# Kernel tuning notes

Measured on AMD Instinct MI355X. Metric: run time of the kernel, lower is better.

Reference implementation:

```python
import jax, jax.numpy as jnp
import numpy as np

T, B = 128, 512
OBS_DIM = 512
HIDDEN = 512
ACTION_DIM = 18
LN_EPS = 1e-6  # flax LayerNorm default


def _layer_norm(x, scale, bias):
    m = jnp.mean(x, axis=-1, keepdims=True)
    v = jnp.var(x, axis=-1, keepdims=True)
    return (x - m) * jax.lax.rsqrt(v + LN_EPS) * scale + bias


def setup_inputs() -> dict:
    key = jax.random.key(0)
    ks = jax.random.split(key, 16)
    sc = lambda k, sh: jax.random.normal(k, sh, jnp.float32) * (1.0 / np.sqrt(sh[0]))
    d = {}
    d['hidden'] = jax.random.normal(ks[0], (B, HIDDEN), jnp.float32)
    d['obs'] = jax.random.normal(ks[1], (T, B, OBS_DIM), jnp.float32)
    d['dones'] = jax.random.randint(ks[2], (T, B), 0, 2).astype(bool)
    d['last_acts'] = jax.random.randint(ks[3], (T, B), 0, ACTION_DIM, dtype=jnp.int32)
    in0 = OBS_DIM + ACTION_DIM
    d['w0'] = sc(ks[4], (in0, HIDDEN)); d['b0'] = jnp.zeros((HIDDEN,), jnp.float32)
    d['ln0_s'] = jnp.ones((HIDDEN,), jnp.float32); d['ln0_b'] = jnp.zeros((HIDDEN,), jnp.float32)
    d['w1'] = sc(ks[5], (HIDDEN, HIDDEN)); d['b1'] = jnp.zeros((HIDDEN,), jnp.float32)
    d['ln1_s'] = jnp.ones((HIDDEN,), jnp.float32); d['ln1_b'] = jnp.zeros((HIDDEN,), jnp.float32)
    d['w_ir'] = sc(ks[6], (HIDDEN, HIDDEN)); d['b_ir'] = jnp.zeros((HIDDEN,), jnp.float32)
    d['w_iz'] = sc(ks[7], (HIDDEN, HIDDEN)); d['b_iz'] = jnp.zeros((HIDDEN,), jnp.float32)
    d['w_in'] = sc(ks[8], (HIDDEN, HIDDEN)); d['b_in'] = jnp.zeros((HIDDEN,), jnp.float32)
    d['w_hr'] = sc(ks[9], (HIDDEN, HIDDEN))
    d['w_hz'] = sc(ks[10], (HIDDEN, HIDDEN))
    d['w_hn'] = sc(ks[11], (HIDDEN, HIDDEN)); d['b_hn'] = jnp.zeros((HIDDEN,), jnp.float32)
    d['w_out'] = sc(ks[12], (HIDDEN, ACTION_DIM)); d['b_out'] = jnp.zeros((ACTION_DIM,), jnp.float32)
    return d


def reference(hidden, obs, dones, last_acts,
              w0, b0, ln0_s, ln0_b, w1, b1, ln1_s, ln1_b,
              w_ir, b_ir, w_iz, b_iz, w_in, b_in,
              w_hr, w_hz, w_hn, b_hn, w_out, b_out):
    # embed last actions and concat with obs: [T, B, obs_dim + action_dim]
    one_hot = jax.nn.one_hot(last_acts, ACTION_DIM, dtype=obs.dtype)
    x = jnp.concatenate([obs, one_hot], axis=-1)
    # MLP encoder: Dense -> LayerNorm -> relu, applied over all (T, B) at once
    x = jax.nn.relu(_layer_norm(x @ w0 + b0, ln0_s, ln0_b))
    x = jax.nn.relu(_layer_norm(x @ w1 + b1, ln1_s, ln1_b))

    # ScannedRNN: GRUCell with reset-to-zero carry on done, scanned over time
    def step(h, xs):
        xt, dt = xs  # xt: [B, H], dt: [B] bool
        h = jnp.where(dt[:, None], jnp.zeros_like(h), h)
        r = jax.nn.sigmoid(xt @ w_ir + b_ir + h @ w_hr)
        z = jax.nn.sigmoid(xt @ w_iz + b_iz + h @ w_hz)
        n = jnp.tanh(xt @ w_in + b_in + r * (h @ w_hn + b_hn))
        h_new = (1.0 - z) * n + z * h
        return h_new, h_new

    new_hidden, y = jax.lax.scan(step, hidden, (x, dones))
    q_vals = y @ w_out + b_out  # [T, B, action_dim]
    return new_hidden, q_vals
```

## Files before the change

### kernel.cpp

```cpp
#include <hip/hip_runtime.h>
#include <cstdint>
#include <cstddef>


#define TT 128
#define BBATCH 512
#define HH 512
#define MM 65536
#define AD 18
#define GSTEPS 8
#define FSTRIDE 32
#define READY_U32 1064960

typedef __attribute__((ext_vector_type(8))) short short8;
typedef __attribute__((ext_vector_type(4))) float float4v;
typedef __attribute__((ext_vector_type(4))) unsigned int uint4v;

__device__ __forceinline__ unsigned short f2bf(float f) {
  union { float f; unsigned int u; } v; v.f = f;
  unsigned int r = v.u + 0x7fffu + ((v.u >> 16) & 1u);
  return (unsigned short)(r >> 16);
}
__device__ __forceinline__ float bf2f(unsigned short h) {
  union { unsigned int u; float f; } v; v.u = ((unsigned int)h) << 16;
  return v.f;
}

__device__ __forceinline__ unsigned int load_u32_coh(const unsigned int* p) {
  unsigned int v;
  asm volatile("global_load_dword %0, %1, off sc0 sc1\n\ts_waitcnt vmcnt(0)"
               : "=v"(v) : "v"(p) : "memory");
  return v;
}
__device__ __forceinline__ void store_u32_coh(unsigned int* p, unsigned int v) {
  asm volatile("global_store_dword %0, %1, off sc0 sc1"
               :: "v"(p), "v"(v) : "memory");
}
__device__ __forceinline__ void store_u64_coh(void* p, unsigned long long v) {
  asm volatile("global_store_dwordx2 %0, %1, off sc0 sc1"
               :: "v"(p), "v"(v) : "memory");
}

typedef __attribute__((address_space(3))) unsigned int* lds_u32p;
typedef const __attribute__((address_space(1))) unsigned int* glb_u32p;
__device__ __forceinline__ void async16(void* lds, const void* g) {
  __builtin_amdgcn_global_load_lds(
      (glb_u32p)(unsigned long long)g,
      (lds_u32p)(unsigned int)(unsigned long long)lds, 16, 0, 0);
}


__global__ __launch_bounds__(256) void k_prep(
    const float* __restrict__ w0, const float* __restrict__ w1,
    const float* __restrict__ wir, const float* __restrict__ wiz,
    const float* __restrict__ win,
    const float* __restrict__ whr, const float* __restrict__ whz,
    const float* __restrict__ whn,
    const float* __restrict__ bir, const float* __restrict__ biz,
    const float* __restrict__ bin, const float* __restrict__ wout,
    const float* __restrict__ hidden, const int* __restrict__ dI,
    unsigned short* __restrict__ W0at, unsigned short* __restrict__ W1t,
    unsigned short* __restrict__ Wit, unsigned short* __restrict__ Whf,
    unsigned short* __restrict__ w0act, float* __restrict__ gib,
    unsigned short* __restrict__ WoutT, unsigned short* __restrict__ hbuf,
    unsigned int* __restrict__ flag) {
  int i = blockIdx.x * 256 + threadIdx.x;
  if (i < 1310720) {
    int o = i & 262143, z = i >> 18;
    int n = o >> 9, k = o & 511;
    const float* s = (z == 0) ? w0 : (z == 1) ? w1 : (z == 2) ? wir
                   : (z == 3) ? wiz : win;
    unsigned short b = f2bf(s[k * 512 + n]);
    if (z == 0) W0at[o] = b;
    else if (z == 1) W1t[o] = b;
    else Wit[(size_t)(z - 2) * 262144 + o] = b;
  } else if (i < 2097152) {
    int j = i - 1310720;
    int k = j / 1536, n = j - k * 1536;
    const float* s = (n < 512) ? whr : (n < 1024) ? whz : whn;
    Whf[((size_t)(k >> 3) * 1536 + n) * 8 + (k & 7)] = f2bf(s[k * 512 + (n & 511)]);
  } else {
    int j = i - 2097152;
    if (j < 9216) {
      int a = j >> 9, n = j & 511;
      w0act[j] = f2bf(w0[(512 + a) * 512 + n]);
    }
    if (j < 1536)
      gib[j] = (j < 512) ? bir[j] : (j < 1024) ? biz[j - 512] : bin[j - 1024];
    if (j < 32768) {
      int n = j >> 9, k = j & 511;
      WoutT[j] = f2bf(n < AD ? wout[k * AD + n] : 0.f);
    }
    hbuf[j] = f2bf(hidden[j]);
  }
  if (blockIdx.x == 9215) {
    __shared__ int wany[4];
    int t = threadIdx.x;
    int any = 0;
#pragma unroll 8
    for (int v = 0; v < 64; ++v) any |= dI[t * 64 + v] & 0xFFFFFFFE;
    unsigned long long b = __ballot(any != 0);
    if ((t & 63) == 0) wany[t >> 6] = (b != 0ull) ? 1 : 0;
    __syncthreads();
    if (t == 0) *flag = (unsigned int)(wany[0] | wany[1] | wany[2] | wany[3]);
  }
}

__global__ __launch_bounds__(256) void k_zero(unsigned int* __restrict__ p) {
  int i = (blockIdx.x * 256 + threadIdx.x) * 4;
  if (i < READY_U32) *(uint4v*)(p + i) = (uint4v){0u, 0u, 0u, 0u};
}


template <int MODE>
__global__ __launch_bounds__(512, 1) void k_enc(
    const unsigned short* __restrict__ Ab,
    const unsigned short* __restrict__ Btb,
    unsigned short* __restrict__ Cb,
    const float* __restrict__ bias,
    const float* __restrict__ lnS, const float* __restrict__ lnB,
    const unsigned short* __restrict__ gW,
    const int* __restrict__ acts) {
  __shared__ __align__(16) unsigned char AsRaw[MODE == 0 ? 32768 : 16384];
  __shared__ unsigned short Bs[32768];
  __shared__ float part[128][4][2];
  __shared__ float stats[128][2];
  float* Asf = (float*)AsRaw;
  unsigned short* Ash = (unsigned short*)AsRaw;

  const int tid = threadIdx.x, wave = tid >> 6, lane = tid & 63;
  const int quad = lane >> 4, l15 = lane & 15;
  const int wm = wave >> 2, wn = wave & 3;
  const int m0 = blockIdx.x * 128;
  const int g = (MODE == 2) ? blockIdx.y : 0;
  const unsigned short* Bt = Btb + (size_t)g * 262144;
  const float* bi = bias + g * 512;

  float4v acc[4][8];
#pragma unroll
  for (int a = 0; a < 4; ++a)
#pragma unroll
    for (int b = 0; b < 8; ++b) acc[a][b] = (float4v){0.f, 0.f, 0.f, 0.f};

  for (int k0 = 0; k0 < 512; k0 += 64) {
    if constexpr (MODE == 0) {
      const float* Af = (const float*)Ab;
#pragma unroll
      for (int r = 0; r < 4; ++r) {
        int u = r * 512 + tid;
        int ch = u >> 8, rem = u & 255, mm = rem >> 1, half = rem & 1;
        async16(&Asf[(size_t)(r * 512 + wave * 64) * 4],
                Af + (size_t)(m0 + mm) * 512 + k0 + ch * 8 + half * 4);
      }
    } else {
#pragma unroll
      for (int r = 0; r < 2; ++r) {
        int u = r * 512 + tid;
        int ch = u >> 7, mm = u & 127;
        async16(&Ash[(size_t)(r * 512 + wave * 64) * 8],
                Ab + (size_t)(m0 + mm) * 512 + k0 + ch * 8);
      }
    }
#pragma unroll
    for (int r = 0; r < 8; ++r) {
      int u = r * 512 + tid;
      int ch = u >> 9, nn = u & 511;
      async16(&Bs[(size_t)(r * 512 + wave * 64) * 8],
              Bt + (size_t)nn * 512 + k0 + ch * 8);
    }
    __syncthreads();
#pragma unroll
    for (int kk = 0; kk < 2; ++kk) {
      short8 afr[4], bfr[8];
#pragma unroll
      for (int mi = 0; mi < 4; ++mi) {
        int mrow = wm * 64 + mi * 16 + l15;
        if constexpr (MODE == 0) {
          const float* ap = &Asf[(size_t)((kk * 4 + quad) * 128 + mrow) * 8];
          float4v lo = *(const float4v*)ap;
          float4v hi = *(const float4v*)(ap + 4);
          short8 f;
#pragma unroll
          for (int j = 0; j < 4; ++j) {
            f[j] = (short)f2bf(lo[j]);
            f[j + 4] = (short)f2bf(hi[j]);
          }
          afr[mi] = f;
        } else {
          afr[mi] = *(const short8*)
              &Ash[(size_t)((kk * 4 + quad) * 128 + mrow) * 8];
        }
      }
#pragma unroll
      for (int ni = 0; ni < 8; ++ni)
        bfr[ni] = *(const short8*)
            &Bs[((kk * 4 + quad) * 512 + wn * 128 + ni * 16 + l15) * 8];
#pragma unroll
      for (int mi = 0; mi < 4; ++mi)
#pragma unroll
        for (int ni = 0; ni < 8; ++ni)
          acc[mi][ni] = __builtin_amdgcn_mfma_f32_16x16x32_bf16(
              afr[mi], bfr[ni], acc[mi][ni], 0, 0, 0);
    }
    __syncthreads();
  }

  float bcol[8];
#pragma unroll
  for (int ni = 0; ni < 8; ++ni) bcol[ni] = bi[wn * 128 + ni * 16 + l15];
#pragma unroll
  for (int mi = 0; mi < 4; ++mi)
#pragma unroll
    for (int i = 0; i < 4; ++i) {
      int row = m0 + wm * 64 + mi * 16 + quad * 4 + i;
      int arow = (MODE == 0) ? acts[row] : 0;
#pragma unroll
      for (int ni = 0; ni < 8; ++ni) {
        float v = acc[mi][ni][i] + bcol[ni];
        if (MODE == 0) v += bf2f(gW[arow * 512 + wn * 128 + ni * 16 + l15]);
        acc[mi][ni][i] = v;
      }
    }

  if (MODE <= 1) {
#pragma unroll
    for (int mi = 0; mi < 4; ++mi)
#pragma unroll
      for (int i = 0; i < 4; ++i) {
        float s = 0.f, q = 0.f;
#pragma unroll
        for (int ni = 0; ni < 8; ++ni) {
          float v = acc[mi][ni][i];
          s += v; q += v * v;
        }
#pragma unroll
        for (int d = 1; d < 16; d <<= 1) {
          s += __shfl_xor(s, d, 64);
          q += __shfl_xor(q, d, 64);
        }
        if (l15 == 0) {
          int rowl = wm * 64 + mi * 16 + quad * 4 + i;
          part[rowl][wn][0] = s;
          part[rowl][wn][1] = q;
        }
      }
    __syncthreads();
    if (tid < 128) {
      float s = part[tid][0][0] + part[tid][1][0] + part[tid][2][0] + part[tid][3][0];
      float q = part[tid][0][1] + part[tid][1][1] + part[tid][2][1] + part[tid][3][1];
      float mean = s * (1.f / 512.f);
      float var = fmaxf(q * (1.f / 512.f) - mean * mean, 0.f);
      stats[tid][0] = mean;
      stats[tid][1] = rsqrtf(var + 1e-6f);
    }
    __syncthreads();
    float sc8[8], cb8[8];
#pragma unroll
    for (int ni = 0; ni < 8; ++ni) {
      int col = wn * 128 + ni * 16 + l15;
      sc8[ni] = lnS[col];
      cb8[ni] = lnB[col];
    }
#pragma unroll
    for (int mi = 0; mi < 4; ++mi)
#pragma unroll
      for (int i = 0; i < 4; ++i) {
        int rowl = wm * 64 + mi * 16 + quad * 4 + i;
        float mean = stats[rowl][0], rstd = stats[rowl][1];
        int row = m0 + rowl;
#pragma unroll
        for (int ni = 0; ni < 8; ++ni) {
          int col = wn * 128 + ni * 16 + l15;
          float v = fmaxf((acc[mi][ni][i] - mean) * rstd * sc8[ni] + cb8[ni], 0.f);
          Cb[(size_t)row * 512 + col] = f2bf(v);
        }
      }
  } else {
#pragma unroll
    for (int mi = 0; mi < 4; ++mi)
#pragma unroll
      for (int i = 0; i < 4; ++i) {
        int row = m0 + wm * 64 + mi * 16 + quad * 4 + i;
        int t = row >> 9, b = row & 511;
#pragma unroll
        for (int ni = 0; ni < 8; ++ni) {
          int c = wn * 128 + ni * 16 + l15;
          size_t dst = ((size_t)((b >> 5) * 16 + (c >> 5)) * 128 + t) * 3072
                     + (size_t)g * 1024 + (b & 31) * 32 + (c & 31);
          Cb[dst] = f2bf(acc[mi][ni][i]);
        }
      }
  }
}


__global__ __launch_bounds__(256, 1) void k_gru(
    const unsigned short* __restrict__ Whf, const unsigned short* __restrict__ gin,
    const float* __restrict__ bhn, const int* __restrict__ dI,
    const unsigned char* __restrict__ dB, const unsigned int* __restrict__ flag,
    const unsigned short* __restrict__ hbuf, unsigned short* __restrict__ ybuf,
    float* __restrict__ outh, unsigned int* __restrict__ ready) {
  __shared__ __align__(16) unsigned short gin_lds[2][GSTEPS * 3 * 32 * 32];
  __shared__ unsigned char d_lds[TT * 32];

  const int tid = threadIdx.x, wave = tid >> 6, lane = tid & 63;
  const int quad = lane >> 4, l15 = lane & 15;
  const int rt = blockIdx.x & 15;
  const int cc = blockIdx.x >> 4;
  const int r0b = rt * 32;
  const int rowb = (wave & 1) * 16 + l15;
  const int row = r0b + rowb;
  const int c0 = cc * 32 + (wave >> 1) * 16 + quad * 4;
  const int bytemode = (int)(*flag);
  const float4v bhn4 = *(const float4v*)(bhn + c0);

  const unsigned short* gsrc = gin + (size_t)(rt * 16 + cc) * 128 * 3072;

  auto stage_gin = [&](int buf, int t0) {
    const unsigned short* src = gsrc + (size_t)t0 * 3072;
#pragma unroll
    for (int r = 0; r < 12; ++r) {
      async16(&gin_lds[buf][(size_t)(r * 256 + wave * 64) * 8],
              src + (size_t)(r * 256 + tid) * 8);
    }
  };

  stage_gin(0, 0);
#pragma unroll
  for (int r = 0; r < 16; ++r) {
    int idx = r * 256 + tid;
    int t = idx >> 5, rr = idx & 31;
    int gidx = t * 512 + r0b + rr;
    d_lds[idx] = bytemode ? dB[gidx] : (unsigned char)(dI[gidx] != 0);
  }

  short8 bw[3][16];
#pragma unroll
  for (int kc = 0; kc < 16; ++kc)
#pragma unroll
    for (int g = 0; g < 3; ++g) {
      size_t u = (size_t)(kc * 4 + quad) * 1536
               + (g * 512 + cc * 32 + (wave >> 1) * 16 + l15);
      bw[g][kc] = *(const short8*)(Whf + u * 8);
    }

  float hprev[4];
  {
    unsigned long long w = *(const unsigned long long*)(hbuf + (size_t)row * 512 + c0);
#pragma unroll
    for (int i = 0; i < 4; ++i) hprev[i] = bf2f((unsigned short)(w >> (16 * i)));
  }

  __syncthreads();

  for (int t = 0; t < TT; ++t) {
    if (t > 0) {
      if (wave == 0) {
        const unsigned int* fp =
            ready + (((size_t)rt * 130 + t) * 16 + (lane & 15)) * FSTRIDE;
        unsigned int v;
        int guard = 0;
        do {
          v = load_u32_coh(fp);
        } while (__ballot(v == 0u) != 0ull && ++guard < (1 << 22));
      }
      __syncthreads();
      asm volatile("" ::: "memory");
    }

    const unsigned short* hsrc =
        (t == 0) ? hbuf : ybuf + (size_t)(t - 1) * 262144;
    const unsigned short* ap = hsrc + (size_t)row * 512 + quad * 8;
    short8 af[16];
#pragma unroll
    for (int kc = 0; kc < 16; ++kc) af[kc] = *(const short8*)(ap + kc * 32);

    const int dd = (int)d_lds[(t << 5) + rowb];
    if (dd) {
      const short8 z8 = {0, 0, 0, 0, 0, 0, 0, 0};
#pragma unroll
      for (int kc = 0; kc < 16; ++kc) af[kc] = z8;
    }

    if ((t & (GSTEPS - 1)) == 0 && t + GSTEPS < TT)
      stage_gin(((t >> 3) + 1) & 1, t + GSTEPS);

    const int sl = t & (GSTEPS - 1), bufc = (t >> 3) & 1;
    float gr[4], gz[4], gn[4];
    {
      const unsigned short* gl = &gin_lds[bufc][(size_t)sl * 3072
          + rowb * 32 + (wave >> 1) * 16 + quad * 4];
      unsigned long long w0 = *(const unsigned long long*)(gl);
      unsigned long long w1 = *(const unsigned long long*)(gl + 1024);
      unsigned long long w2 = *(const unsigned long long*)(gl + 2048);
#pragma unroll
      for (int i = 0; i < 4; ++i) {
        gr[i] = bf2f((unsigned short)(w0 >> (16 * i)));
        gz[i] = bf2f((unsigned short)(w1 >> (16 * i)));
        gn[i] = bf2f((unsigned short)(w2 >> (16 * i)));
      }
    }

    float4v a0 = {0.f, 0.f, 0.f, 0.f}, a1 = a0, a2 = a0;
#pragma unroll
    for (int kc = 0; kc < 16; ++kc) {
      a0 = __builtin_amdgcn_mfma_f32_16x16x32_bf16(bw[0][kc], af[kc], a0, 0, 0, 0);
      a1 = __builtin_amdgcn_mfma_f32_16x16x32_bf16(bw[1][kc], af[kc], a1, 0, 0, 0);
      a2 = __builtin_amdgcn_mfma_f32_16x16x32_bf16(bw[2][kc], af[kc], a2, 0, 0, 0);
    }

    unsigned short* ydst = ybuf + (size_t)t * 262144;
    float hv[4];
#pragma unroll
    for (int i = 0; i < 4; ++i) {
      float hold = dd ? 0.f : hprev[i];
      float r = 1.f / (1.f + __expf(-(a0[i] + gr[i])));
      float z = 1.f / (1.f + __expf(-(a1[i] + gz[i])));
      float npre = gn[i] + r * (a2[i] + bhn4[i]);
      float n = 1.f - 2.f / (1.f + __expf(2.f * npre));
      hv[i] = (1.f - z) * n + z * hold;
      hprev[i] = hv[i];
    }
    {
      unsigned long long pk = (unsigned long long)f2bf(hv[0])
          | ((unsigned long long)f2bf(hv[1]) << 16)
          | ((unsigned long long)f2bf(hv[2]) << 32)
          | ((unsigned long long)f2bf(hv[3]) << 48);
      store_u64_coh(ydst + (size_t)row * 512 + c0, pk);
    }
    if (t == TT - 1) {
      float4v o = {hv[0], hv[1], hv[2], hv[3]};
      *(float4v*)(outh + (size_t)row * 512 + c0) = o;
    }

    __syncthreads();
    if (tid == 0)
      store_u32_coh(&ready[(((size_t)rt * 130 + t + 1) * 16 + cc) * FSTRIDE], 1u);
  }
}


__global__ __launch_bounds__(256) void k_qout(
    const unsigned short* __restrict__ Yb, const unsigned short* __restrict__ Wt,
    const float* __restrict__ bout, float* __restrict__ Q) {
  __shared__ unsigned short As[8192];
  __shared__ unsigned short Bs[4096];
  const int tid = threadIdx.x, wave = tid >> 6, lane = tid & 63;
  const int quad = lane >> 4, l15 = lane & 15;
  const int m0 = blockIdx.x * 128;

  float4v acc[2][4];
#pragma unroll
  for (int a = 0; a < 2; ++a)
#pragma unroll
    for (int b = 0; b < 4; ++b) acc[a][b] = (float4v){0.f, 0.f, 0.f, 0.f};

  for (int k0 = 0; k0 < 512; k0 += 64) {
#pragma unroll
    for (int r = 0; r < 4; ++r) {
      int u = r * 256 + wave * 64 + lane;
      int ch = u >> 7, mm = u & 127;
      async16(&As[(size_t)(r * 256 + wave * 64) * 8],
              Yb + (size_t)(m0 + mm) * 512 + k0 + ch * 8);
    }
#pragma unroll
    for (int r = 0; r < 2; ++r) {
      int u = r * 256 + wave * 64 + lane;
      int ch = u >> 6, nn = u & 63;
      async16(&Bs[(size_t)(r * 256 + wave * 64) * 8],
              Wt + (size_t)nn * 512 + k0 + ch * 8);
    }
    __syncthreads();
#pragma unroll
    for (int kk = 0; kk < 2; ++kk) {
      short8 afr[2], bfr[4];
#pragma unroll
      for (int mi = 0; mi < 2; ++mi)
        afr[mi] = *(const short8*)
            &As[((kk * 4 + quad) * 128 + wave * 32 + mi * 16 + l15) * 8];
#pragma unroll
      for (int ni = 0; ni < 4; ++ni)
        bfr[ni] = *(const short8*)
            &Bs[((kk * 4 + quad) * 64 + ni * 16 + l15) * 8];
#pragma unroll
      for (int mi = 0; mi < 2; ++mi)
#pragma unroll
        for (int ni = 0; ni < 4; ++ni)
          acc[mi][ni] = __builtin_amdgcn_mfma_f32_16x16x32_bf16(
              afr[mi], bfr[ni], acc[mi][ni], 0, 0, 0);
    }
    __syncthreads();
  }
#pragma unroll
  for (int mi = 0; mi < 2; ++mi)
#pragma unroll
    for (int ni = 0; ni < 4; ++ni)
#pragma unroll
      for (int i = 0; i < 4; ++i) {
        int row = m0 + wave * 32 + mi * 16 + quad * 4 + i;
        int colq = ni * 16 + l15;
        if (colq < AD) Q[(size_t)row * AD + colq] = acc[mi][ni][i] + bout[colq];
      }
}


extern "C" void kernel_launch(void* const* d_in, const int* in_sizes, int n_in,
                              void* d_out, int out_size, void* d_ws,
                              size_t ws_size, hipStream_t stream) {
  const float* hidden = (const float*)d_in[0];
  const float* obs = (const float*)d_in[1];
  const void* dones = d_in[2];
  const int* acts = (const int*)d_in[3];
  const float* w0 = (const float*)d_in[4];
  const float* b0 = (const float*)d_in[5];
  const float* ln0s = (const float*)d_in[6];
  const float* ln0b = (const float*)d_in[7];
  const float* w1 = (const float*)d_in[8];
  const float* b1 = (const float*)d_in[9];
  const float* ln1s = (const float*)d_in[10];
  const float* ln1b = (const float*)d_in[11];
  const float* wir = (const float*)d_in[12];
  const float* bir = (const float*)d_in[13];
  const float* wiz = (const float*)d_in[14];
  const float* biz = (const float*)d_in[15];
  const float* win = (const float*)d_in[16];
  const float* bin = (const float*)d_in[17];
  const float* whr = (const float*)d_in[18];
  const float* whz = (const float*)d_in[19];
  const float* whn = (const float*)d_in[20];
  const float* bhn = (const float*)d_in[21];
  const float* wout = (const float*)d_in[22];
  const float* bout = (const float*)d_in[23];

  char* ws = (char*)d_ws;
  unsigned short* bufA = (unsigned short*)(ws);
  unsigned short* bufB = (unsigned short*)(ws + 67108864ULL);
  unsigned short* gin = (unsigned short*)(ws + 134217728ULL);
  char* D = ws + 134217728ULL + 201326592ULL;
  unsigned short* W0at = (unsigned short*)(D);
  unsigned short* W1t = (unsigned short*)(D + 524288);
  unsigned short* Wit = (unsigned short*)(D + 1048576);
  unsigned short* Whf = (unsigned short*)(D + 2621440);
  unsigned short* WoutT = (unsigned short*)(D + 4194304);
  unsigned short* w0act = (unsigned short*)(D + 4259840);
  float* gib = (float*)(D + 4292608);
  unsigned short* hbuf = (unsigned short*)(D + 4300800);
  unsigned int* flag = (unsigned int*)(D + 4825088);
  unsigned int* ready = (unsigned int*)ws;

  (void)in_sizes; (void)n_in; (void)out_size; (void)ws_size;

  k_prep<<<9216, 256, 0, stream>>>(w0, w1, wir, wiz, win, whr, whz, whn,
                                   bir, biz, bin, wout, hidden,
                                   (const int*)dones, W0at, W1t, Wit, Whf,
                                   w0act, gib, WoutT, hbuf, flag);
  k_enc<0><<<512, 512, 0, stream>>>((const unsigned short*)obs, W0at, bufB,
                                    b0, ln0s, ln0b, w0act, acts);
  k_enc<1><<<512, 512, 0, stream>>>(bufB, W1t, bufA, b1, ln1s, ln1b,
                                    nullptr, nullptr);
  k_enc<2><<<dim3(512, 3), 512, 0, stream>>>(bufA, Wit, gin, gib, nullptr,
                                             nullptr, nullptr, nullptr);
  k_zero<<<1041, 256, 0, stream>>>(ready);
  k_gru<<<256, 256, 0, stream>>>(Whf, gin, bhn, (const int*)dones,
                                 (const unsigned char*)dones, flag, hbuf, bufB,
                                 (float*)d_out, ready);
  k_qout<<<512, 256, 0, stream>>>(bufB, WoutT, bout, (float*)d_out + 262144);
}
```

Measured before the change: 1.209 ms.

## Replace ready-flag handshake with poisoned-data polling in GRU recurrence

The per-step flag array and its zeroing kernel are removed. The output buffer is now pre-filled with an all-ones poison pattern, and each GRU block spins directly on its h-row loads until no bf16 element equals 0xFFFF. This removes the flag store and flag poll round trip on every timestep, at the cost of writing a 64MB poison fill and re-issuing loads while polling. Correctness depends on no real hidden value encoding to 0xFFFF (a NaN pattern) and on the 16-byte stores being observed atomically.

```diff
diff --git a/kernel.cpp b/kernel.cpp
--- a/kernel.cpp
+++ b/kernel.cpp
@@ -9,8 +9,6 @@
 #define MM 65536
 #define AD 18
 #define GSTEPS 8
-#define FSTRIDE 32
-#define READY_U32 1064960
 
 typedef __attribute__((ext_vector_type(8))) short short8;
 typedef __attribute__((ext_vector_type(4))) float float4v;
@@ -26,19 +24,15 @@
   return v.f;
 }
 
-__device__ __forceinline__ unsigned int load_u32_coh(const unsigned int* p) {
-  unsigned int v;
-  asm volatile("global_load_dword %0, %1, off sc0 sc1\n\ts_waitcnt vmcnt(0)"
-               : "=v"(v) : "v"(p) : "memory");
-  return v;
-}
-__device__ __forceinline__ void store_u32_coh(unsigned int* p, unsigned int v) {
-  asm volatile("global_store_dword %0, %1, off sc0 sc1"
-               :: "v"(p), "v"(v) : "memory");
-}
 __device__ __forceinline__ void store_u64_coh(void* p, unsigned long long v) {
   asm volatile("global_store_dwordx2 %0, %1, off sc0 sc1"
                :: "v"(p), "v"(v) : "memory");
+}
+__device__ __forceinline__ short8 load16_coh(const unsigned short* p) {
+  short8 v;
+  asm volatile("global_load_dwordx4 %0, %1, off sc0 sc1"
+               : "=v"(v) : "v"(p));
+  return v;
 }
 
 typedef __attribute__((address_space(3))) unsigned int* lds_u32p;
@@ -106,9 +100,9 @@
   }
 }
 
-__global__ __launch_bounds__(256) void k_zero(unsigned int* __restrict__ p) {
-  int i = (blockIdx.x * 256 + threadIdx.x) * 4;
-  if (i < READY_U32) *(uint4v*)(p + i) = (uint4v){0u, 0u, 0u, 0u};
+__global__ __launch_bounds__(256) void k_pois(uint4v* __restrict__ p) {
+  p[(size_t)blockIdx.x * 256 + threadIdx.x] =
+      (uint4v){0xFFFFFFFFu, 0xFFFFFFFFu, 0xFFFFFFFFu, 0xFFFFFFFFu};
 }
 
 
@@ -299,7 +293,7 @@
     const float* __restrict__ bhn, const int* __restrict__ dI,
     const unsigned char* __restrict__ dB, const unsigned int* __restrict__ flag,
     const unsigned short* __restrict__ hbuf, unsigned short* __restrict__ ybuf,
-    float* __restrict__ outh, unsigned int* __restrict__ ready) {
+    float* __restrict__ outh) {
   __shared__ __align__(16) unsigned short gin_lds[2][GSTEPS * 3 * 32 * 32];
   __shared__ unsigned char d_lds[TT * 32];
 
@@ -354,26 +348,31 @@
   __syncthreads();
 
   for (int t = 0; t < TT; ++t) {
-    if (t > 0) {
-      if (wave == 0) {
-        const unsigned int* fp =
-            ready + (((size_t)rt * 130 + t) * 16 + (lane & 15)) * FSTRIDE;
-        unsigned int v;
-        int guard = 0;
-        do {
-          v = load_u32_coh(fp);
-        } while (__ballot(v == 0u) != 0ull && ++guard < (1 << 22));
-      }
-      __syncthreads();
-      asm volatile("" ::: "memory");
-    }
-
     const unsigned short* hsrc =
         (t == 0) ? hbuf : ybuf + (size_t)(t - 1) * 262144;
     const unsigned short* ap = hsrc + (size_t)row * 512 + quad * 8;
     short8 af[16];
-#pragma unroll
-    for (int kc = 0; kc < 16; ++kc) af[kc] = *(const short8*)(ap + kc * 32);
+    unsigned valid = 0;
+    int guard = 0;
+    do {
+#pragma unroll
+      for (int kc = 0; kc < 16; ++kc)
+        if (!(valid & (1u << kc))) af[kc] = load16_coh(ap + kc * 32);
+      asm volatile("s_waitcnt vmcnt(0)" ::: "memory");
+      __builtin_amdgcn_sched_barrier(0);
+#pragma unroll
+      for (int kc = 0; kc < 16; ++kc)
+        if (!(valid & (1u << kc))) {
+          uint4v u = *(uint4v*)&af[kc];
+          unsigned bad = 0;
+#pragma unroll
+          for (int j = 0; j < 4; ++j) {
+            unsigned a = u[j];
+            bad |= ((a & 0xFFFFu) == 0xFFFFu) | ((a >> 16) == 0xFFFFu);
+          }
+          valid |= bad ? 0u : (1u << kc);
+        }
+    } while (__ballot(valid != 0xFFFFu) != 0ull && ++guard < (1 << 20));
 
     const int dd = (int)d_lds[(t << 5) + rowb];
     if (dd) {
@@ -434,8 +433,6 @@
     }
 
     __syncthreads();
-    if (tid == 0)
-      store_u32_coh(&ready[(((size_t)rt * 130 + t + 1) * 16 + cc) * FSTRIDE], 1u);
   }
 }
 
@@ -546,7 +543,6 @@
   float* gib = (float*)(D + 4292608);
   unsigned short* hbuf = (unsigned short*)(D + 4300800);
   unsigned int* flag = (unsigned int*)(D + 4825088);
-  unsigned int* ready = (unsigned int*)ws;
 
   (void)in_sizes; (void)n_in; (void)out_size; (void)ws_size;
 
@@ -558,11 +554,11 @@
                                     b0, ln0s, ln0b, w0act, acts);
   k_enc<1><<<512, 512, 0, stream>>>(bufB, W1t, bufA, b1, ln1s, ln1b,
                                     nullptr, nullptr);
+  k_pois<<<16384, 256, 0, stream>>>((uint4v*)bufB);
   k_enc<2><<<dim3(512, 3), 512, 0, stream>>>(bufA, Wit, gin, gib, nullptr,
                                              nullptr, nullptr, nullptr);
-  k_zero<<<1041, 256, 0, stream>>>(ready);
   k_gru<<<256, 256, 0, stream>>>(Whf, gin, bhn, (const int*)dones,
                                  (const unsigned char*)dones, flag, hbuf, bufB,
-                                 (float*)d_out, ready);
+                                 (float*)d_out);
   k_qout<<<512, 256, 0, stream>>>(bufB, WoutT, bout, (float*)d_out + 262144);
 }
```

After: 1.374 ms. 1.14x slower.
